# Kernel optimization log

Measured on AMD Instinct MI355X. Metric: run time of the kernel, lower is better.

## Reference

```python
import jax, jax.numpy as jnp
import numpy as np

B, N = 32768, 512

def setup_inputs() -> dict:
    key = jax.random.key(0)
    k1, k2, k3, k4 = jax.random.split(key, 4)
    log_sigma_hat = jax.random.normal(k1, (B, N), dtype=jnp.float32)
    sigma = jax.random.normal(k2, (B, N), dtype=jnp.float32)
    SR = jax.random.normal(k3, (N,), dtype=jnp.float32)
    # well-conditioned invertible Gamma (covariance-like): A A^T / N + I
    A = jax.random.normal(k4, (N, N), dtype=jnp.float32)
    Gamma = A @ A.T / N + jnp.eye(N, dtype=jnp.float32)
    return {"log_sigma_hat": log_sigma_hat, "sigma": sigma, "SR": SR, "Gamma": Gamma, "k": 12}

def reference(log_sigma_hat, sigma, SR, Gamma, k):
    # r[t] = exp(sigma[t]) / exp(log_sigma_hat[t])  -> [B, N]
    r = jnp.exp(sigma - log_sigma_hat)
    Gamma_inv = jnp.linalg.inv(Gamma)
    v = Gamma_inv @ SR           # [N]  Gamma^{-1} SR
    u = Gamma_inv.T @ SR         # [N]  (SR^T Gamma^{-1})^T
    # first  = SR^T Gamma^{-1} diag(r) SR / k = sum(u * r * SR)
    first = (r * (u * SR)).sum(axis=-1) / k
    # second = SR^T Gamma^{-1} diag(r) Gamma diag(r) Gamma^{-1} SR / (2k)
    w = r * v                                     # [B, N] = diag(r) v
    Gw = jnp.einsum('ij,bj->bi', Gamma, w)        # [B, N] = Gamma diag(r) v
    second = (u * (r * Gw)).sum(axis=-1) / (2 * k)
    utils = first - second                        # [B]
    return -utils.mean()
```

## Files before the change

### kernel.cpp

```cpp
#include <hip/hip_runtime.h>
#include <hip/hip_bf16.h>
#include <stdint.h>

#define BB 32768
#define NN 512
#define CG1 4
#define CG2 3
#define NPART 64
#define NTILE 10

typedef __attribute__((ext_vector_type(8))) short bf16x8;
typedef __attribute__((ext_vector_type(4))) float f32x4;

__device__ __forceinline__ void gld_lds16(const void* g, void* l) {
  typedef __attribute__((address_space(1))) const unsigned int gas_u32;
  typedef __attribute__((address_space(3))) unsigned int las_u32;
  __builtin_amdgcn_global_load_lds((gas_u32*)(uintptr_t)g,
                                   (las_u32*)(uint32_t)(uintptr_t)l, 16, 0, 0);
}

__device__ __forceinline__ unsigned short f2bf(float x) {
  __hip_bfloat16 h = __float2bfloat16(x);
  return *reinterpret_cast<unsigned short*>(&h);
}

__device__ __forceinline__ float bf2f(unsigned short u) {
  return __uint_as_float(((unsigned)u) << 16);
}

__device__ __forceinline__ float wave_reduce(float v) {
#pragma unroll
  for (int off = 32; off > 0; off >>= 1) v += __shfl_xor(v, off, 64);
  return v;
}

__device__ __forceinline__ float block_reduce(float v, float* red) {
  v = wave_reduce(v);
  const int wv = threadIdx.x >> 6, ln = threadIdx.x & 63;
  if (ln == 0) red[wv] = v;
  __syncthreads();
  if (threadIdx.x == 0) {
    float a = 0;
#pragma unroll
    for (int i = 0; i < 8; ++i) a += red[i];
    red[8] = a;
  }
  __syncthreads();
  return red[8];
}

__device__ void cg_phase(const unsigned short* __restrict__ Gbf, const float* __restrict__ SR,
                         float* __restrict__ st, float* __restrict__ v_out,
                         float* sm, int first, int iters) {
  float* sp = sm;
  float* apw = sm + 512;
  float* red = sm + 2560;
  const int t = threadIdx.x;
  const int rg = t >> 7;
  const int c0 = (t & 127) * 4;
  float x, r, p, rr;
  if (first) {
    float s = SR[t];
    x = 0.f; r = s; p = s;
    rr = block_reduce(s * s, red);
  } else {
    x = st[t]; r = st[512 + t]; p = st[1024 + t]; rr = st[1536];
  }
  for (int it = 0; it < iters; ++it) {
    sp[t] = p;
    __syncthreads();
    float a0 = 0, a1 = 0, a2 = 0, a3 = 0;
    for (int j = 0; j < NN; j += 32) {
#pragma unroll
      for (int jj = 0; jj < 8; ++jj) {
        const int row = j + jj * 4 + rg;
        ushort4 u = *(const ushort4*)(Gbf + row * NN + c0);
        float pv = sp[row];
        a0 += bf2f(u.x) * pv; a1 += bf2f(u.y) * pv;
        a2 += bf2f(u.z) * pv; a3 += bf2f(u.w) * pv;
      }
    }
    *(float4*)(apw + rg * 512 + c0) = make_float4(a0, a1, a2, a3);
    __syncthreads();
    float ap = apw[t] + apw[512 + t] + apw[1024 + t] + apw[1536 + t];
    float pAp = block_reduce(p * ap, red);
    float alpha = rr / pAp;
    x += alpha * p;
    r -= alpha * ap;
    float rrn = block_reduce(r * r, red);
    float beta = rrn / rr;
    p = r + beta * p;
    rr = rrn;
    __syncthreads();
  }
  if (v_out) {
    v_out[t] = x;
  } else {
    st[t] = x; st[512 + t] = r; st[1024 + t] = p;
    if (t == 0) st[1536] = rr;
  }
}

__global__ __launch_bounds__(256) void k0_prep(
    const float* __restrict__ Gam, unsigned short* __restrict__ Gbf,
    float* __restrict__ small_zero) {
  const int t = threadIdx.x, b = blockIdx.x;
  const size_t base = ((size_t)b * 256 + t) * 8;
  float4 g0 = *(const float4*)(Gam + base);
  float4 g1 = *(const float4*)(Gam + base + 4);
  *(ushort4*)(Gbf + base) = make_ushort4(f2bf(g0.x), f2bf(g0.y), f2bf(g0.z), f2bf(g0.w));
  *(ushort4*)(Gbf + base + 4) = make_ushort4(f2bf(g1.x), f2bf(g1.y), f2bf(g1.z), f2bf(g1.w));
  if (b == 0)
    for (int i = t; i < 4160; i += 256) small_zero[i] = 0.f;
}

__global__ __launch_bounds__(512) void k1_rexp(
    const float* __restrict__ lsh, const float* __restrict__ sig,
    const float* __restrict__ SR, const unsigned short* __restrict__ Gbf,
    unsigned short* __restrict__ Rt, float* __restrict__ colsum,
    float* __restrict__ cgst) {
  __shared__ __align__(16) float sm[3392];
  if (blockIdx.x == 0) {
    cg_phase(Gbf, SR, cgst, nullptr, sm, 1, CG1);
    return;
  }
  unsigned short* tile = (unsigned short*)sm;
  float* scr = sm + 1152;
  const int t = threadIdx.x;
  const int tc = t & 15, tg = t >> 4;
  const int wb = blockIdx.x - 1;
  const int bb = wb * 32;
  const int jl = t >> 3, bc = (t & 7) * 4;
  for (int jt = 0; jt < 8; ++jt) {
    const int j0 = jt * 64;
    const size_t off = (size_t)(bb + tg) * NN + j0 + 4 * tc;
    float4 sv = *(const float4*)(sig + off);
    float4 lv = *(const float4*)(lsh + off);
    float r0 = __expf(sv.x - lv.x), r1 = __expf(sv.y - lv.y);
    float r2 = __expf(sv.z - lv.z), r3 = __expf(sv.w - lv.w);
    scr[tg * 68 + 4 * tc + 0] = r0;
    scr[tg * 68 + 4 * tc + 1] = r1;
    scr[tg * 68 + 4 * tc + 2] = r2;
    scr[tg * 68 + 4 * tc + 3] = r3;
    tile[(4 * tc + 0) * 36 + tg] = f2bf(r0);
    tile[(4 * tc + 1) * 36 + tg] = f2bf(r1);
    tile[(4 * tc + 2) * 36 + tg] = f2bf(r2);
    tile[(4 * tc + 3) * 36 + tg] = f2bf(r3);
    __syncthreads();
    {
      ushort4 vv = *(const ushort4*)(tile + jl * 36 + bc);
      *(ushort4*)(Rt + (size_t)(j0 + jl) * BB + bb + bc) = vv;
    }
    if (t < 64) {
      float s = 0;
#pragma unroll
      for (int g = 0; g < 32; ++g) s += scr[g * 68 + t];
      atomicAdd(&colsum[(wb & 7) * NN + j0 + t], s);
    }
    __syncthreads();
  }
}

__global__ __launch_bounds__(512) void k2_syrk(
    const unsigned short* __restrict__ Rt, const unsigned short* __restrict__ Gbf,
    unsigned short* __restrict__ Cpart, float* __restrict__ cgst,
    float* __restrict__ v_out) {
  __shared__ __align__(16) unsigned short smem[16384];
  if (blockIdx.x == 0) {
    cg_phase(Gbf, nullptr, cgst, v_out, (float*)smem, 0, CG2);
    return;
  }
  const int wb = blockIdx.x - 1;
  const int kc = wb / NTILE, tt = wb % NTILE;
  const int ti = (int)((0x3221110000ULL >> (4 * tt)) & 0xF);
  const int tj = (int)((0x3323213210ULL >> (4 * tt)) & 0xF);
  const int i0 = ti * 128, j0 = tj * 128;
  const int diag = (ti == tj);
  const size_t b0 = (size_t)kc * 512;
  const int t = threadIdx.x, lane = t & 63, wv = t >> 6;
  const int wi = (wv & 3) * 32, wj = (wv >> 2) * 64;
  const int lm = lane & 15, lq = lane >> 4;
  unsigned short* As = smem;
  unsigned short* Bs = diag ? smem : smem + 8192;
  const int srow = t >> 3, scol = (t & 7) * 8;
  f32x4 acc[2][4];
#pragma unroll
  for (int a = 0; a < 2; ++a)
#pragma unroll
    for (int b = 0; b < 4; ++b) acc[a][b] = (f32x4){0.f, 0.f, 0.f, 0.f};

  for (int ks = 0; ks < 8; ++ks) {
    const size_t bcur = b0 + ks * 64;
    gld_lds16(Rt + (size_t)(i0 + srow) * BB + bcur + scol, As + srow * 64 + scol);
    gld_lds16(Rt + (size_t)(i0 + 64 + srow) * BB + bcur + scol, As + (64 + srow) * 64 + scol);
    if (!diag) {
      gld_lds16(Rt + (size_t)(j0 + srow) * BB + bcur + scol, Bs + srow * 64 + scol);
      gld_lds16(Rt + (size_t)(j0 + 64 + srow) * BB + bcur + scol, Bs + (64 + srow) * 64 + scol);
    }
    __syncthreads();
#pragma unroll
    for (int s = 0; s < 2; ++s) {
      bf16x8 af[2], bfr[4];
#pragma unroll
      for (int g = 0; g < 2; ++g)
        af[g] = *(const bf16x8*)(As + (wi + g * 16 + lm) * 64 + s * 32 + lq * 8);
#pragma unroll
      for (int g = 0; g < 4; ++g)
        bfr[g] = *(const bf16x8*)(Bs + (wj + g * 16 + lm) * 64 + s * 32 + lq * 8);
#pragma unroll
      for (int gm = 0; gm < 2; ++gm)
#pragma unroll
        for (int gn = 0; gn < 4; ++gn)
          acc[gm][gn] = __builtin_amdgcn_mfma_f32_16x16x32_bf16(af[gm], bfr[gn], acc[gm][gn], 0, 0, 0);
    }
    __syncthreads();
  }
  unsigned short* Cw = Cpart + (size_t)kc * NN * NN;
#pragma unroll
  for (int gm = 0; gm < 2; ++gm) {
    const int rbase = i0 + wi + gm * 16 + lq * 4;
#pragma unroll
    for (int gn = 0; gn < 4; ++gn) {
      const int col = j0 + wj + gn * 16 + lm;
      unsigned short e0 = f2bf(acc[gm][gn][0]), e1 = f2bf(acc[gm][gn][1]);
      unsigned short e2 = f2bf(acc[gm][gn][2]), e3 = f2bf(acc[gm][gn][3]);
      Cw[(size_t)(rbase + 0) * NN + col] = e0;
      Cw[(size_t)(rbase + 1) * NN + col] = e1;
      Cw[(size_t)(rbase + 2) * NN + col] = e2;
      Cw[(size_t)(rbase + 3) * NN + col] = e3;
      if (!diag)
        *(ushort4*)(Cw + (size_t)col * NN + rbase) = make_ushort4(e0, e1, e2, e3);
    }
  }
}

__global__ __launch_bounds__(256) void k3_contract(
    const float* __restrict__ Gamma, const unsigned short* __restrict__ Cpart,
    const float* __restrict__ v, float* __restrict__ secondsum) {
  __shared__ float red[4];
  const int t = threadIdx.x;
  const size_t e = ((size_t)blockIdx.x * 256 + t) * 4;
  const int i = (int)(e >> 9), j = (int)(e & 511);
  float cx = 0, cy = 0, cz = 0, cw = 0;
  for (int pp = 0; pp < NPART; ++pp) {
    ushort4 u = *(const ushort4*)(Cpart + (size_t)pp * NN * NN + e);
    cx += bf2f(u.x); cy += bf2f(u.y); cz += bf2f(u.z); cw += bf2f(u.w);
  }
  float4 g = *(const float4*)(Gamma + e);
  float4 vj = *(const float4*)(v + j);
  float vi = v[i];
  float p = vi * (g.x * cx * vj.x + g.y * cy * vj.y + g.z * cz * vj.z + g.w * cw * vj.w);
  p = wave_reduce(p);
  if ((t & 63) == 0) red[t >> 6] = p;
  __syncthreads();
  if (t == 0) atomicAdd(secondsum, red[0] + red[1] + red[2] + red[3]);
}

__global__ __launch_bounds__(512) void k4_final(
    const float* __restrict__ colsum, const float* __restrict__ v,
    const float* __restrict__ SR, const float* __restrict__ secondsum,
    const int* __restrict__ kp, float* __restrict__ out) {
  __shared__ float red[8];
  const int t = threadIdx.x;
  float cs = 0;
#pragma unroll
  for (int bk = 0; bk < 8; ++bk) cs += colsum[bk * NN + t];
  float f = (cs * (1.0f / BB)) * v[t] * SR[t];
  f = wave_reduce(f);
  if ((t & 63) == 0) red[t >> 6] = f;
  __syncthreads();
  if (t == 0) {
    float first = 0;
#pragma unroll
    for (int i = 0; i < 8; ++i) first += red[i];
    float kk = (float)kp[0];
    float sec = secondsum[0] / ((float)BB * 2.0f * kk);
    out[0] = -(first / kk - sec);
  }
}

extern "C" void kernel_launch(void* const* d_in, const int* in_sizes, int n_in,
                              void* d_out, int out_size, void* d_ws, size_t ws_size,
                              hipStream_t stream) {
  const float* lsh = (const float*)d_in[0];
  const float* sig = (const float*)d_in[1];
  const float* SR = (const float*)d_in[2];
  const float* Gam = (const float*)d_in[3];
  const int* kp = (const int*)d_in[4];
  char* ws = (char*)d_ws;
  unsigned short* Cpart = (unsigned short*)ws;
  const size_t coff = (size_t)NPART * NN * NN * sizeof(unsigned short);
  float* colsum = (float*)(ws + coff);
  float* secsum = colsum + 4096;
  float* cgst = secsum + 64;
  float* v = cgst + 1664;
  unsigned short* Gbf = (unsigned short*)(ws + coff + (32 << 10));
  unsigned short* Rt = (unsigned short*)(ws + coff + (32 << 10) + (512 << 10));

  k0_prep<<<128, 256, 0, stream>>>(Gam, Gbf, colsum);
  k1_rexp<<<1025, 512, 0, stream>>>(lsh, sig, SR, Gbf, Rt, colsum, cgst);
  k2_syrk<<<641, 512, 0, stream>>>(Rt, Gbf, Cpart, cgst, v);
  k3_contract<<<256, 256, 0, stream>>>(Gam, Cpart, v, secsum);
  k4_final<<<1, 512, 0, stream>>>(colsum, v, SR, secsum, kp, (float*)d_out);
}
```

Before: 228.7 us.

## Fuse Gamma-v contraction into SYRK epilogue and drop partial C buffer

The SYRK kernel now contracts its accumulator tile directly against Gamma and v and atomically adds a scalar. This removes the 64 bf16 partial 512x512 matrices and the separate contraction kernel that re-read them. Column sums of r move from the exp/transpose kernel into the diagonal SYRK tiles, read from LDS. The transpose kernel uses 64-row tiles with packed 16-byte stores, the SYRK LDS layout gets an XOR swizzle, and CG now runs all 7 iterations in one block of the first kernel. Risks are serial CG latency in that block and extra atomics on a single scalar.

Result: slower. 244.7 us (+7.0%).

```diff
diff --git a/kernel.cpp b/kernel.cpp
--- a/kernel.cpp
+++ b/kernel.cpp
@@ -4,10 +4,8 @@
 
 #define BB 32768
 #define NN 512
-#define CG1 4
-#define CG2 3
-#define NPART 64
 #define NTILE 10
+#define TSTRIDE 132
 
 typedef __attribute__((ext_vector_type(8))) short bf16x8;
 typedef __attribute__((ext_vector_type(4))) float f32x4;
@@ -50,22 +48,16 @@
 }
 
 __device__ void cg_phase(const unsigned short* __restrict__ Gbf, const float* __restrict__ SR,
-                         float* __restrict__ st, float* __restrict__ v_out,
-                         float* sm, int first, int iters) {
+                         float* __restrict__ v_out, float* sm, int iters) {
   float* sp = sm;
   float* apw = sm + 512;
   float* red = sm + 2560;
   const int t = threadIdx.x;
   const int rg = t >> 7;
   const int c0 = (t & 127) * 4;
-  float x, r, p, rr;
-  if (first) {
-    float s = SR[t];
-    x = 0.f; r = s; p = s;
-    rr = block_reduce(s * s, red);
-  } else {
-    x = st[t]; r = st[512 + t]; p = st[1024 + t]; rr = st[1536];
-  }
+  float s = SR[t];
+  float x = 0.f, r = s, p = s;
+  float rr = block_reduce(s * s, red);
   for (int it = 0; it < iters; ++it) {
     sp[t] = p;
     __syncthreads();
@@ -93,12 +85,7 @@
     rr = rrn;
     __syncthreads();
   }
-  if (v_out) {
-    v_out[t] = x;
-  } else {
-    st[t] = x; st[512 + t] = r; st[1024 + t] = p;
-    if (t == 0) st[1536] = rr;
-  }
+  v_out[t] = x;
 }
 
 __global__ __launch_bounds__(256) void k0_prep(
@@ -117,60 +104,64 @@
 __global__ __launch_bounds__(512) void k1_rexp(
     const float* __restrict__ lsh, const float* __restrict__ sig,
     const float* __restrict__ SR, const unsigned short* __restrict__ Gbf,
-    unsigned short* __restrict__ Rt, float* __restrict__ colsum,
-    float* __restrict__ cgst) {
-  __shared__ __align__(16) float sm[3392];
+    unsigned short* __restrict__ Rt, float* __restrict__ v_out) {
+  __shared__ __align__(16) float sm[4224];
   if (blockIdx.x == 0) {
-    cg_phase(Gbf, SR, cgst, nullptr, sm, 1, CG1);
+    cg_phase(Gbf, SR, v_out, sm, 7);
     return;
   }
   unsigned short* tile = (unsigned short*)sm;
-  float* scr = sm + 1152;
   const int t = threadIdx.x;
-  const int tc = t & 15, tg = t >> 4;
-  const int wb = blockIdx.x - 1;
-  const int bb = wb * 32;
-  const int jl = t >> 3, bc = (t & 7) * 4;
-  for (int jt = 0; jt < 8; ++jt) {
-    const int j0 = jt * 64;
-    const size_t off = (size_t)(bb + tg) * NN + j0 + 4 * tc;
-    float4 sv = *(const float4*)(sig + off);
-    float4 lv = *(const float4*)(lsh + off);
-    float r0 = __expf(sv.x - lv.x), r1 = __expf(sv.y - lv.y);
-    float r2 = __expf(sv.z - lv.z), r3 = __expf(sv.w - lv.w);
-    scr[tg * 68 + 4 * tc + 0] = r0;
-    scr[tg * 68 + 4 * tc + 1] = r1;
-    scr[tg * 68 + 4 * tc + 2] = r2;
-    scr[tg * 68 + 4 * tc + 3] = r3;
-    tile[(4 * tc + 0) * 36 + tg] = f2bf(r0);
-    tile[(4 * tc + 1) * 36 + tg] = f2bf(r1);
-    tile[(4 * tc + 2) * 36 + tg] = f2bf(r2);
-    tile[(4 * tc + 3) * 36 + tg] = f2bf(r3);
-    __syncthreads();
-    {
-      ushort4 vv = *(const ushort4*)(tile + jl * 36 + bc);
-      *(ushort4*)(Rt + (size_t)(j0 + jl) * BB + bb + bc) = vv;
-    }
-    if (t < 64) {
-      float s = 0;
-#pragma unroll
-      for (int g = 0; g < 32; ++g) s += scr[g * 68 + t];
-      atomicAdd(&colsum[(wb & 7) * NN + j0 + t], s);
-    }
-    __syncthreads();
+  const int r = t >> 3, cg = t & 7;
+  const int jr = t >> 3, cc = t & 7;
+  const size_t bb = (size_t)(blockIdx.x - 1) * 64;
+  for (int jt = 0; jt < 4; ++jt) {
+    const int j0 = jt * 128;
+    const size_t off = (bb + r) * NN + j0 + cg * 16;
+    float4 s0 = *(const float4*)(sig + off);
+    float4 s1 = *(const float4*)(sig + off + 4);
+    float4 s2 = *(const float4*)(sig + off + 8);
+    float4 s3 = *(const float4*)(sig + off + 12);
+    float4 l0 = *(const float4*)(lsh + off);
+    float4 l1 = *(const float4*)(lsh + off + 4);
+    float4 l2 = *(const float4*)(lsh + off + 8);
+    float4 l3 = *(const float4*)(lsh + off + 12);
+    ushort4 w0 = make_ushort4(f2bf(__expf(s0.x - l0.x)), f2bf(__expf(s0.y - l0.y)),
+                              f2bf(__expf(s0.z - l0.z)), f2bf(__expf(s0.w - l0.w)));
+    ushort4 w1 = make_ushort4(f2bf(__expf(s1.x - l1.x)), f2bf(__expf(s1.y - l1.y)),
+                              f2bf(__expf(s1.z - l1.z)), f2bf(__expf(s1.w - l1.w)));
+    ushort4 w2 = make_ushort4(f2bf(__expf(s2.x - l2.x)), f2bf(__expf(s2.y - l2.y)),
+                              f2bf(__expf(s2.z - l2.z)), f2bf(__expf(s2.w - l2.w)));
+    ushort4 w3 = make_ushort4(f2bf(__expf(s3.x - l3.x)), f2bf(__expf(s3.y - l3.y)),
+                              f2bf(__expf(s3.z - l3.z)), f2bf(__expf(s3.w - l3.w)));
+    if (jt) __syncthreads();
+    *(ushort4*)(&tile[r * TSTRIDE + cg * 16 + 0]) = w0;
+    *(ushort4*)(&tile[r * TSTRIDE + cg * 16 + 4]) = w1;
+    *(ushort4*)(&tile[r * TSTRIDE + cg * 16 + 8]) = w2;
+    *(ushort4*)(&tile[r * TSTRIDE + cg * 16 + 12]) = w3;
+    __syncthreads();
+#pragma unroll
+    for (int pass = 0; pass < 2; ++pass) {
+      const int j = jr + pass * 64;
+      unsigned int u[4];
+#pragma unroll
+      for (int q = 0; q < 4; ++q) {
+        unsigned int lo = tile[(cc * 8 + 2 * q) * TSTRIDE + j];
+        unsigned int hi = tile[(cc * 8 + 2 * q + 1) * TSTRIDE + j];
+        u[q] = lo | (hi << 16);
+      }
+      *(uint4*)(Rt + (size_t)(j0 + j) * BB + bb + cc * 8) =
+          make_uint4(u[0], u[1], u[2], u[3]);
+    }
   }
 }
 
 __global__ __launch_bounds__(512) void k2_syrk(
-    const unsigned short* __restrict__ Rt, const unsigned short* __restrict__ Gbf,
-    unsigned short* __restrict__ Cpart, float* __restrict__ cgst,
-    float* __restrict__ v_out) {
+    const unsigned short* __restrict__ Rt, const float* __restrict__ Gam,
+    const float* __restrict__ v, float* __restrict__ colsum,
+    float* __restrict__ secsum) {
   __shared__ __align__(16) unsigned short smem[16384];
-  if (blockIdx.x == 0) {
-    cg_phase(Gbf, nullptr, cgst, v_out, (float*)smem, 0, CG2);
-    return;
-  }
-  const int wb = blockIdx.x - 1;
+  const int wb = blockIdx.x;
   const int kc = wb / NTILE, tt = wb % NTILE;
   const int ti = (int)((0x3221110000ULL >> (4 * tt)) & 0xF);
   const int tj = (int)((0x3323213210ULL >> (4 * tt)) & 0xF);
@@ -180,22 +171,26 @@
   const int t = threadIdx.x, lane = t & 63, wv = t >> 6;
   const int wi = (wv & 3) * 32, wj = (wv >> 2) * 64;
   const int lm = lane & 15, lq = lane >> 4;
+  const int xr = lm & 7;
   unsigned short* As = smem;
   unsigned short* Bs = diag ? smem : smem + 8192;
-  const int srow = t >> 3, scol = (t & 7) * 8;
+  const int srow = t >> 3, sc = t & 7;
+  const int scol = (sc ^ (srow & 7)) * 8;
   f32x4 acc[2][4];
 #pragma unroll
   for (int a = 0; a < 2; ++a)
 #pragma unroll
     for (int b = 0; b < 4; ++b) acc[a][b] = (f32x4){0.f, 0.f, 0.f, 0.f};
+  float csum = 0.f;
+  const int crow = t >> 2, cq = t & 3;
 
   for (int ks = 0; ks < 8; ++ks) {
     const size_t bcur = b0 + ks * 64;
-    gld_lds16(Rt + (size_t)(i0 + srow) * BB + bcur + scol, As + srow * 64 + scol);
-    gld_lds16(Rt + (size_t)(i0 + 64 + srow) * BB + bcur + scol, As + (64 + srow) * 64 + scol);
+    gld_lds16(Rt + (size_t)(i0 + srow) * BB + bcur + scol, As + srow * 64 + sc * 8);
+    gld_lds16(Rt + (size_t)(i0 + 64 + srow) * BB + bcur + scol, As + (64 + srow) * 64 + sc * 8);
     if (!diag) {
-      gld_lds16(Rt + (size_t)(j0 + srow) * BB + bcur + scol, Bs + srow * 64 + scol);
-      gld_lds16(Rt + (size_t)(j0 + 64 + srow) * BB + bcur + scol, Bs + (64 + srow) * 64 + scol);
+      gld_lds16(Rt + (size_t)(j0 + srow) * BB + bcur + scol, Bs + srow * 64 + sc * 8);
+      gld_lds16(Rt + (size_t)(j0 + 64 + srow) * BB + bcur + scol, Bs + (64 + srow) * 64 + sc * 8);
     }
     __syncthreads();
 #pragma unroll
@@ -203,57 +198,60 @@
       bf16x8 af[2], bfr[4];
 #pragma unroll
       for (int g = 0; g < 2; ++g)
-        af[g] = *(const bf16x8*)(As + (wi + g * 16 + lm) * 64 + s * 32 + lq * 8);
+        af[g] = *(const bf16x8*)(As + (wi + g * 16 + lm) * 64 + ((s * 4 + lq) ^ xr) * 8);
 #pragma unroll
       for (int g = 0; g < 4; ++g)
-        bfr[g] = *(const bf16x8*)(Bs + (wj + g * 16 + lm) * 64 + s * 32 + lq * 8);
+        bfr[g] = *(const bf16x8*)(Bs + (wj + g * 16 + lm) * 64 + ((s * 4 + lq) ^ xr) * 8);
 #pragma unroll
       for (int gm = 0; gm < 2; ++gm)
 #pragma unroll
         for (int gn = 0; gn < 4; ++gn)
           acc[gm][gn] = __builtin_amdgcn_mfma_f32_16x16x32_bf16(af[gm], bfr[gn], acc[gm][gn], 0, 0, 0);
     }
-    __syncthreads();
-  }
-  unsigned short* Cw = Cpart + (size_t)kc * NN * NN;
+    if (diag) {
+#pragma unroll
+      for (int h = 0; h < 2; ++h) {
+        const int ccs = ((2 * cq + h) ^ (crow & 7)) * 8;
+        const bf16x8 xv = *(const bf16x8*)(As + crow * 64 + ccs);
+#pragma unroll
+        for (int e = 0; e < 8; ++e) csum += bf2f((unsigned short)xv[e]);
+      }
+    }
+    __syncthreads();
+  }
+  if (diag) {
+    float c2 = csum + __shfl_xor(csum, 1, 64);
+    c2 += __shfl_xor(c2, 2, 64);
+    if (cq == 0) atomicAdd(&colsum[(kc & 7) * NN + i0 + crow], c2);
+  }
+  float s_ = 0.f;
 #pragma unroll
   for (int gm = 0; gm < 2; ++gm) {
-    const int rbase = i0 + wi + gm * 16 + lq * 4;
+    const int rb = i0 + wi + gm * 16 + lq * 4;
+    const float vr0 = v[rb], vr1 = v[rb + 1], vr2 = v[rb + 2], vr3 = v[rb + 3];
 #pragma unroll
     for (int gn = 0; gn < 4; ++gn) {
-      const int col = j0 + wj + gn * 16 + lm;
-      unsigned short e0 = f2bf(acc[gm][gn][0]), e1 = f2bf(acc[gm][gn][1]);
-      unsigned short e2 = f2bf(acc[gm][gn][2]), e3 = f2bf(acc[gm][gn][3]);
-      Cw[(size_t)(rbase + 0) * NN + col] = e0;
-      Cw[(size_t)(rbase + 1) * NN + col] = e1;
-      Cw[(size_t)(rbase + 2) * NN + col] = e2;
-      Cw[(size_t)(rbase + 3) * NN + col] = e3;
-      if (!diag)
-        *(ushort4*)(Cw + (size_t)col * NN + rbase) = make_ushort4(e0, e1, e2, e3);
-    }
-  }
-}
-
-__global__ __launch_bounds__(256) void k3_contract(
-    const float* __restrict__ Gamma, const unsigned short* __restrict__ Cpart,
-    const float* __restrict__ v, float* __restrict__ secondsum) {
-  __shared__ float red[4];
-  const int t = threadIdx.x;
-  const size_t e = ((size_t)blockIdx.x * 256 + t) * 4;
-  const int i = (int)(e >> 9), j = (int)(e & 511);
-  float cx = 0, cy = 0, cz = 0, cw = 0;
-  for (int pp = 0; pp < NPART; ++pp) {
-    ushort4 u = *(const ushort4*)(Cpart + (size_t)pp * NN * NN + e);
-    cx += bf2f(u.x); cy += bf2f(u.y); cz += bf2f(u.z); cw += bf2f(u.w);
-  }
-  float4 g = *(const float4*)(Gamma + e);
-  float4 vj = *(const float4*)(v + j);
-  float vi = v[i];
-  float p = vi * (g.x * cx * vj.x + g.y * cy * vj.y + g.z * cz * vj.z + g.w * cw * vj.w);
-  p = wave_reduce(p);
-  if ((t & 63) == 0) red[t >> 6] = p;
-  __syncthreads();
-  if (t == 0) atomicAdd(secondsum, red[0] + red[1] + red[2] + red[3]);
+      const int cl = j0 + wj + gn * 16 + lm;
+      const float vc = v[cl];
+      const float* gp = Gam + (size_t)rb * NN + cl;
+      s_ += acc[gm][gn][0] * gp[0] * vr0 * vc;
+      s_ += acc[gm][gn][1] * gp[NN] * vr1 * vc;
+      s_ += acc[gm][gn][2] * gp[2 * NN] * vr2 * vc;
+      s_ += acc[gm][gn][3] * gp[3 * NN] * vr3 * vc;
+    }
+  }
+  if (!diag) s_ *= 2.f;
+  s_ = wave_reduce(s_);
+  __syncthreads();
+  float* red = (float*)smem;
+  if (lane == 0) red[wv] = s_;
+  __syncthreads();
+  if (t == 0) {
+    float a = 0;
+#pragma unroll
+    for (int i = 0; i < 8; ++i) a += red[i];
+    atomicAdd(secsum, a);
+  }
 }
 
 __global__ __launch_bounds__(512) void k4_final(
@@ -288,18 +286,14 @@
   const float* Gam = (const float*)d_in[3];
   const int* kp = (const int*)d_in[4];
   char* ws = (char*)d_ws;
-  unsigned short* Cpart = (unsigned short*)ws;
-  const size_t coff = (size_t)NPART * NN * NN * sizeof(unsigned short);
-  float* colsum = (float*)(ws + coff);
+  float* colsum = (float*)ws;
   float* secsum = colsum + 4096;
-  float* cgst = secsum + 64;
-  float* v = cgst + 1664;
-  unsigned short* Gbf = (unsigned short*)(ws + coff + (32 << 10));
-  unsigned short* Rt = (unsigned short*)(ws + coff + (32 << 10) + (512 << 10));
+  float* v = secsum + 64;
+  unsigned short* Gbf = (unsigned short*)(ws + (32 << 10));
+  unsigned short* Rt = (unsigned short*)(ws + (32 << 10) + (512 << 10));
 
   k0_prep<<<128, 256, 0, stream>>>(Gam, Gbf, colsum);
-  k1_rexp<<<1025, 512, 0, stream>>>(lsh, sig, SR, Gbf, Rt, colsum, cgst);
-  k2_syrk<<<641, 512, 0, stream>>>(Rt, Gbf, Cpart, cgst, v);
-  k3_contract<<<256, 256, 0, stream>>>(Gam, Cpart, v, secsum);
+  k1_rexp<<<513, 512, 0, stream>>>(lsh, sig, SR, Gbf, Rt, v);
+  k2_syrk<<<640, 512, 0, stream>>>(Rt, Gam, v, colsum, secsum);
   k4_final<<<1, 512, 0, stream>>>(colsum, v, SR, secsum, kp, (float*)d_out);
 }
```
